# Performance work log

Measured on AMD Instinct MI355X. Metric: run time of the kernel, lower is better.

The kernel has to match this reference:

```python
import jax, jax.numpy as jnp
import numpy as np

N_NODES = 50000
N_EDGES = 800000


def setup_inputs() -> dict:
    key = jax.random.key(0)
    ks = jax.random.split(key, 8)
    x = jax.random.normal(ks[0], (N_NODES, 128), dtype=jnp.float32)
    edge_index = jax.random.randint(ks[1], (2, N_EDGES), 0, N_NODES, dtype=jnp.int32)
    # Glorot-ish scaled weights
    W1 = jax.random.normal(ks[2], (128, 64), dtype=jnp.float32) / np.sqrt(128.0)
    b1 = jnp.zeros((64,), dtype=jnp.float32)
    W2 = jax.random.normal(ks[3], (64, 64), dtype=jnp.float32) / np.sqrt(64.0)
    b2 = jnp.zeros((64,), dtype=jnp.float32)
    W3 = jax.random.normal(ks[4], (64, 32), dtype=jnp.float32) / np.sqrt(64.0)
    b3 = jnp.zeros((32,), dtype=jnp.float32)
    return {"x": x, "edge_index": edge_index, "W1": W1, "b1": b1,
            "W2": W2, "b2": b2, "W3": W3, "b3": b3}


def _gcn_norm(edge_index, n_nodes):
    """Add self-loops and compute symmetric GCN edge normalization."""
    loop = jnp.arange(n_nodes, dtype=edge_index.dtype)
    src = jnp.concatenate([edge_index[0], loop])  # [E+N]
    dst = jnp.concatenate([edge_index[1], loop])
    deg = jax.ops.segment_sum(jnp.ones_like(dst, dtype=jnp.float32), dst,
                              num_segments=n_nodes)
    dis = jax.lax.rsqrt(jnp.maximum(deg, 1.0))  # deg >= 1 due to self-loops
    norm = dis[src] * dis[dst]                  # [E+N]
    return src, dst, norm


def _gcn_conv(h, W, b, src, dst, norm, n_nodes):
    # transform-then-aggregate (PyG GCNConv): messages have out_channels dim
    h = h @ W                                   # [N, out]
    msg = h[src] * norm[:, None]                # [E+N, out] gather + scale
    out = jax.ops.segment_sum(msg, dst, num_segments=n_nodes)  # scatter-add
    return out + b


def reference(x, edge_index, W1, b1, W2, b2, W3, b3):
    n = x.shape[0]
    src, dst, norm = _gcn_norm(edge_index, n)
    h = jax.nn.relu(_gcn_conv(x, W1, b1, src, dst, norm, n))
    # dropout is identity in eval mode
    h = jax.nn.relu(_gcn_conv(h, W2, b2, src, dst, norm, n))
    out = _gcn_conv(h, W3, b3, src, dst, norm, n)
    return out
```

## Files before the change

kernel.cpp:

```cpp
#include <hip/hip_runtime.h>
#include <hip/hip_fp16.h>


#define P3CAP 3200
#define P4CAP 8192

typedef float vf4 __attribute__((ext_vector_type(4)));

__device__ __forceinline__ int block_scan_incl(int v, int* s, int t) {
    s[t] = v;
    __syncthreads();
#pragma unroll
    for (int d = 1; d < 256; d <<= 1) {
        int a = (t >= d) ? s[t - d] : 0;
        __syncthreads();
        s[t] += a;
        __syncthreads();
    }
    return s[t];
}

__host__ __device__ __forceinline__ int chunk_of(int E) {
    return (((E + 255) / 256) + 3) & ~3;
}

__global__ __launch_bounds__(256) void part_hist_kernel(
    const int* __restrict__ dst, int* __restrict__ hist, int E, int nbuckets)
{
    __shared__ int lh[256];
    const int t = threadIdx.x;
    lh[t] = 0;
    __syncthreads();
    const int chunk = chunk_of(E);
    const int e0 = blockIdx.x * chunk;
    const int e1 = min(E, e0 + chunk);
    int e = e0 + t * 4;
    for (; e + 3 < e1; e += 1024) {
        const int4 d4 = *(const int4*)&dst[e];
        atomicAdd(&lh[d4.x >> 8], 1);
        atomicAdd(&lh[d4.y >> 8], 1);
        atomicAdd(&lh[d4.z >> 8], 1);
        atomicAdd(&lh[d4.w >> 8], 1);
    }
    for (; e < e1; ++e) atomicAdd(&lh[dst[e] >> 8], 1);
    __syncthreads();
    if (t < nbuckets) hist[t * 256 + blockIdx.x] = lh[t];
}

__global__ __launch_bounds__(256) void part_scan_kernel(
    int* __restrict__ hist, int* __restrict__ btot)
{
    __shared__ int s[256];
    const int t = threadIdx.x;
    const int v = hist[blockIdx.x * 256 + t];
    const int inc = block_scan_incl(v, s, t);
    hist[blockIdx.x * 256 + t] = inc - v;
    if (t == 255) btot[blockIdx.x] = inc;
}

__global__ __launch_bounds__(256) void part_scatter_kernel(
    const int* __restrict__ src, const int* __restrict__ dst,
    const int* __restrict__ hist, const int* __restrict__ btot,
    int* __restrict__ bedge, int E, int nbuckets)
{
    __shared__ int lh[256], gb[256], cur[256], s[256];
    __shared__ int stage[P3CAP];
    const int t = threadIdx.x;

    const int bv = (t < nbuckets) ? btot[t] : 0;
    const int binc = block_scan_incl(bv, s, t);
    const int bbase_t = binc - bv;
    __syncthreads();

    lh[t] = 0;
    __syncthreads();
    const int chunk = chunk_of(E);
    const int e0 = blockIdx.x * chunk;
    const int e1 = min(E, e0 + chunk);
    {
        int e = e0 + t * 4;
        for (; e + 3 < e1; e += 1024) {
            const int4 d4 = *(const int4*)&dst[e];
            atomicAdd(&lh[d4.x >> 8], 1);
            atomicAdd(&lh[d4.y >> 8], 1);
            atomicAdd(&lh[d4.z >> 8], 1);
            atomicAdd(&lh[d4.w >> 8], 1);
        }
        for (; e < e1; ++e) atomicAdd(&lh[dst[e] >> 8], 1);
    }
    __syncthreads();
    const int v = lh[t];
    const int inc = block_scan_incl(v, s, t);
    const int excl = inc - v;
    cur[t] = excl;
    if (t < nbuckets) gb[t] = bbase_t + hist[t * 256 + blockIdx.x] - excl;
    __syncthreads();
    {
        int e = e0 + t * 4;
        for (; e + 3 < e1; e += 1024) {
            const int4 d4 = *(const int4*)&dst[e];
            const int4 s4 = *(const int4*)&src[e];
            int r, b;
            b = d4.x >> 8; r = atomicAdd(&cur[b], 1);
            stage[r] = (s4.x & 0xffff) | ((d4.x & 255) << 16) | (b << 24);
            b = d4.y >> 8; r = atomicAdd(&cur[b], 1);
            stage[r] = (s4.y & 0xffff) | ((d4.y & 255) << 16) | (b << 24);
            b = d4.z >> 8; r = atomicAdd(&cur[b], 1);
            stage[r] = (s4.z & 0xffff) | ((d4.z & 255) << 16) | (b << 24);
            b = d4.w >> 8; r = atomicAdd(&cur[b], 1);
            stage[r] = (s4.w & 0xffff) | ((d4.w & 255) << 16) | (b << 24);
        }
        for (; e < e1; ++e) {
            const int dv = dst[e];
            const int b = dv >> 8;
            const int r = atomicAdd(&cur[b], 1);
            stage[r] = (src[e] & 0xffff) | ((dv & 255) << 16) | (b << 24);
        }
    }
    __syncthreads();
    const int cnt = e1 - e0;
    for (int i = t; i < cnt; i += 256) {
        const int p = stage[i];
        const int bucket = (int)((unsigned)p >> 24);
        bedge[gb[bucket] + i] = p;
    }
}

__global__ __launch_bounds__(256) void bucket_csr_kernel(
    const int* __restrict__ bedge, const int* __restrict__ btot,
    int* __restrict__ csr, int* __restrict__ off, float* __restrict__ dis,
    int N, int nbuckets)
{
    __shared__ int deg[256], cur[256], s[256];
    __shared__ int e01[2];
    __shared__ int lcsr[P4CAP];
    const int t = threadIdx.x;
    const int b = blockIdx.x;

    const int bv = (t < nbuckets) ? btot[t] : 0;
    const int binc = block_scan_incl(bv, s, t);
    if (t == b) { e01[0] = binc - bv; e01[1] = binc; }
    __syncthreads();
    const int e0 = e01[0], e1 = e01[1];

    deg[t] = 0;
    __syncthreads();
    for (int e = e0 + t; e < e1; e += 256)
        atomicAdd(&deg[(bedge[e] >> 16) & 255], 1);
    __syncthreads();
    const int v = deg[t];
    const int inc = block_scan_incl(v, s, t);
    cur[t] = inc - v;
    const int node = (b << 8) + t;
    if (node < N) {
        off[node + 1] = e0 + inc;
        dis[node] = rsqrtf((float)v + 1.0f);
        if (node == 0) off[0] = 0;
    }
    __syncthreads();
    for (int e = e0 + t; e < e1; e += 256) {
        const int p = bedge[e];
        const int pos = atomicAdd(&cur[(p >> 16) & 255], 1);
        lcsr[pos] = p & 0xffff;
    }
    __syncthreads();
    for (int i = t; i < e1 - e0; i += 256)
        csr[e0 + i] = lcsr[i];
}

template<int K, int C, int TR>
__global__ __launch_bounds__(256) void gemm_scale_kernel(
    const float* __restrict__ in, const float* __restrict__ W,
    const float* __restrict__ dis, __half* __restrict__ hp, int N)
{
    constexpr int TX = C / 4;
    constexpr int R  = (256 / TX) * TR;
    __shared__ float Wl[K * C];

    const int t = threadIdx.x;
    for (int i = t; i < K * C / 4; i += 256)
        ((float4*)Wl)[i] = ((const float4*)W)[i];
    __syncthreads();

    const int tx = t % TX, ty = t / TX;
    const int cb = tx * 4;
    const int row0 = blockIdx.x * R + ty * TR;

    float acc[TR][4];
#pragma unroll
    for (int r = 0; r < TR; ++r) acc[r][0] = acc[r][1] = acc[r][2] = acc[r][3] = 0.0f;

    auto store_row = [&](int row, int r) {
        const float d = dis[row];
        __half2 h0 = __float22half2_rn(make_float2(acc[r][0] * d, acc[r][1] * d));
        __half2 h1 = __float22half2_rn(make_float2(acc[r][2] * d, acc[r][3] * d));
        uint2 u;
        u.x = *(unsigned*)&h0;
        u.y = *(unsigned*)&h1;
        *(uint2*)&hp[(size_t)row * C + cb] = u;
    };

    if (row0 + TR <= N) {
        const float* inp = in + (size_t)row0 * K;
#pragma unroll 4
        for (int k4 = 0; k4 < K / 4; ++k4) {
            float4 w0 = *(const float4*)&Wl[(k4 * 4 + 0) * C + cb];
            float4 w1 = *(const float4*)&Wl[(k4 * 4 + 1) * C + cb];
            float4 w2 = *(const float4*)&Wl[(k4 * 4 + 2) * C + cb];
            float4 w3 = *(const float4*)&Wl[(k4 * 4 + 3) * C + cb];
#pragma unroll
            for (int r = 0; r < TR; ++r) {
                const vf4 a = __builtin_nontemporal_load((const vf4*)&inp[r * K + k4 * 4]);
                acc[r][0] = fmaf(a.x, w0.x, acc[r][0]);
                acc[r][1] = fmaf(a.x, w0.y, acc[r][1]);
                acc[r][2] = fmaf(a.x, w0.z, acc[r][2]);
                acc[r][3] = fmaf(a.x, w0.w, acc[r][3]);
                acc[r][0] = fmaf(a.y, w1.x, acc[r][0]);
                acc[r][1] = fmaf(a.y, w1.y, acc[r][1]);
                acc[r][2] = fmaf(a.y, w1.z, acc[r][2]);
                acc[r][3] = fmaf(a.y, w1.w, acc[r][3]);
                acc[r][0] = fmaf(a.z, w2.x, acc[r][0]);
                acc[r][1] = fmaf(a.z, w2.y, acc[r][1]);
                acc[r][2] = fmaf(a.z, w2.z, acc[r][2]);
                acc[r][3] = fmaf(a.z, w2.w, acc[r][3]);
                acc[r][0] = fmaf(a.w, w3.x, acc[r][0]);
                acc[r][1] = fmaf(a.w, w3.y, acc[r][1]);
                acc[r][2] = fmaf(a.w, w3.z, acc[r][2]);
                acc[r][3] = fmaf(a.w, w3.w, acc[r][3]);
            }
        }
#pragma unroll
        for (int r = 0; r < TR; ++r) store_row(row0 + r, r);
    } else {
        for (int k = 0; k < K; ++k) {
            const float4 w4 = *(const float4*)&Wl[k * C + cb];
#pragma unroll
            for (int r = 0; r < TR; ++r) {
                const int row = row0 + r;
                const float a = (row < N) ? in[(size_t)row * K + k] : 0.0f;
                acc[r][0] = fmaf(a, w4.x, acc[r][0]);
                acc[r][1] = fmaf(a, w4.y, acc[r][1]);
                acc[r][2] = fmaf(a, w4.z, acc[r][2]);
                acc[r][3] = fmaf(a, w4.w, acc[r][3]);
            }
        }
#pragma unroll
        for (int r = 0; r < TR; ++r)
            if (row0 + r < N) store_row(row0 + r, r);
    }
}

template<int COUT>
__global__ __launch_bounds__(256) void fused_agg_gemm_kernel(
    const int* __restrict__ off, const int* __restrict__ csr,
    const float* __restrict__ dis, const __half* __restrict__ hp_in,
    const float* __restrict__ bias, const float* __restrict__ Wn,
    __half* __restrict__ hp_out, int N)
{
    constexpr int TX  = COUT / 4;
    constexpr int NPB = 256 / TX;
    constexpr int NPW = NPB / 4;
    __shared__ float Wl[64 * COUT];
    __shared__ float Al[NPB * 65];

    const int t = threadIdx.x;
    for (int i = t; i < 64 * COUT / 4; i += 256)
        ((float4*)Wl)[i] = ((const float4*)Wn)[i];

    const int wv   = t >> 6;
    const int lane = t & 63;
    const int grp  = lane >> 3;
    const int gl   = lane & 7;

    float b[8];
#pragma unroll
    for (int j = 0; j < 8; ++j) b[j] = bias[gl * 8 + j];

    auto accum = [](float4 v, float* a) {
        const __half2* h2 = (const __half2*)&v;
#pragma unroll
        for (int j = 0; j < 4; ++j) {
            const float2 pr = __half22float2(h2[j]);
            a[2 * j]     += pr.x;
            a[2 * j + 1] += pr.y;
        }
    };

    const int node0 = blockIdx.x * NPB + wv * NPW;
    for (int nl = 0; nl < NPW; ++nl) {
        const int node = node0 + nl;
        if (node >= N) break;
        const int s0 = off[node];
        const int s1 = off[node + 1];

        float acc[8]  = {0, 0, 0, 0, 0, 0, 0, 0};
        float acc2[8] = {0, 0, 0, 0, 0, 0, 0, 0};

        if (grp == 0) {
            const float4 v = *(const float4*)&hp_in[(size_t)node * 64 + gl * 8];
            accum(v, acc);
        }
        int e = s0 + grp;
        for (; e + 8 < s1; e += 16) {
            const int sa = csr[e];
            const int sb = csr[e + 8];
            const float4 va = *(const float4*)&hp_in[(size_t)sa * 64 + gl * 8];
            const float4 vb = *(const float4*)&hp_in[(size_t)sb * 64 + gl * 8];
            accum(va, acc);
            accum(vb, acc2);
        }
        if (e < s1) {
            const int sa = csr[e];
            const float4 va = *(const float4*)&hp_in[(size_t)sa * 64 + gl * 8];
            accum(va, acc);
        }
#pragma unroll
        for (int j = 0; j < 8; ++j) acc[j] += acc2[j];
#pragma unroll
        for (int d = 8; d < 64; d <<= 1) {
#pragma unroll
            for (int j = 0; j < 8; ++j) acc[j] += __shfl_xor(acc[j], d);
        }
        if (grp == 0) {
            const float dn = dis[node];
            const int row = wv * NPW + nl;
#pragma unroll
            for (int j = 0; j < 8; ++j)
                Al[row * 65 + gl * 8 + j] = fmaxf(fmaf(dn, acc[j], b[j]), 0.0f);
        }
    }
    __syncthreads();

    const int tx = t % TX, ty = t / TX;
    const int gnode = blockIdx.x * NPB + ty;
    const int cb = tx * 4;
    float c0 = 0.f, c1 = 0.f, c2 = 0.f, c3 = 0.f;
#pragma unroll 8
    for (int k = 0; k < 64; ++k) {
        const float a = Al[ty * 65 + k];
        const float4 w4 = *(const float4*)&Wl[k * COUT + cb];
        c0 = fmaf(a, w4.x, c0);
        c1 = fmaf(a, w4.y, c1);
        c2 = fmaf(a, w4.z, c2);
        c3 = fmaf(a, w4.w, c3);
    }
    if (gnode < N) {
        const float d = dis[gnode];
        __half2 h0 = __float22half2_rn(make_float2(c0 * d, c1 * d));
        __half2 h1 = __float22half2_rn(make_float2(c2 * d, c3 * d));
        uint2 u;
        u.x = *(unsigned*)&h0;
        u.y = *(unsigned*)&h1;
        *(uint2*)&hp_out[(size_t)gnode * COUT + cb] = u;
    }
}

template<int C, bool RELU>
__global__ __launch_bounds__(256) void agg_kernel(
    const int* __restrict__ off, const int* __restrict__ csr,
    const float* __restrict__ dis, const __half* __restrict__ hp,
    const float* __restrict__ bias, float* __restrict__ out, int N)
{
    constexpr int GL = C / 8;
    constexpr int G  = 64 / GL;
    const int wv   = threadIdx.x >> 6;
    const int lane = threadIdx.x & 63;
    const int grp  = lane / GL;
    const int gl   = lane % GL;
    const int node = blockIdx.x * 4 + wv;
    if (node >= N) return;

    const int s0 = off[node];
    const int s1 = off[node + 1];

    float acc[8]  = {0, 0, 0, 0, 0, 0, 0, 0};
    float acc2[8] = {0, 0, 0, 0, 0, 0, 0, 0};

    auto accum = [](float4 v, float* a) {
        const __half2* h2 = (const __half2*)&v;
#pragma unroll
        for (int j = 0; j < 4; ++j) {
            const float2 pr = __half22float2(h2[j]);
            a[2 * j]     += pr.x;
            a[2 * j + 1] += pr.y;
        }
    };

    if (grp == 0) {
        const float4 v = *(const float4*)&hp[(size_t)node * C + gl * 8];
        accum(v, acc);
    }
    int e = s0 + grp;
    for (; e + G < s1; e += 2 * G) {
        const int sa = csr[e];
        const int sb = csr[e + G];
        const float4 va = *(const float4*)&hp[(size_t)sa * C + gl * 8];
        const float4 vb = *(const float4*)&hp[(size_t)sb * C + gl * 8];
        accum(va, acc);
        accum(vb, acc2);
    }
    if (e < s1) {
        const int sa = csr[e];
        const float4 va = *(const float4*)&hp[(size_t)sa * C + gl * 8];
        accum(va, acc);
    }
#pragma unroll
    for (int j = 0; j < 8; ++j) acc[j] += acc2[j];

#pragma unroll
    for (int d = GL; d < 64; d <<= 1) {
#pragma unroll
        for (int j = 0; j < 8; ++j) acc[j] += __shfl_xor(acc[j], d);
    }

    if (grp == 0) {
        const float dn = dis[node];
        float v[8];
#pragma unroll
        for (int j = 0; j < 8; ++j) {
            v[j] = fmaf(dn, acc[j], bias[gl * 8 + j]);
            if (RELU) v[j] = fmaxf(v[j], 0.f);
        }
        *(float4*)&out[(size_t)node * C + gl * 8]     = make_float4(v[0], v[1], v[2], v[3]);
        *(float4*)&out[(size_t)node * C + gl * 8 + 4] = make_float4(v[4], v[5], v[6], v[7]);
    }
}

static inline size_t align_up(size_t x) { return (x + 255) & ~(size_t)255; }

extern "C" void kernel_launch(void* const* d_in, const int* in_sizes, int n_in,
                              void* d_out, int out_size, void* d_ws, size_t ws_size,
                              hipStream_t stream) {
    const float* x   = (const float*)d_in[0];
    const int*  eidx = (const int*)d_in[1];
    const float* W1  = (const float*)d_in[2];
    const float* b1  = (const float*)d_in[3];
    const float* W2  = (const float*)d_in[4];
    const float* b2  = (const float*)d_in[5];
    const float* W3  = (const float*)d_in[6];
    const float* b3  = (const float*)d_in[7];
    float* out = (float*)d_out;

    const int N = in_sizes[0] / 128;
    const int E = in_sizes[1] / 2;
    const int* srcp = eidx;
    const int* dstp = eidx + E;
    const int nbuckets = (N + 255) >> 8;

    char* ws = (char*)d_ws;
    size_t o = 0;
    float* dis   = (float*)(ws + o);  o = align_up(o + (size_t)N * 4);
    int* off     = (int*)(ws + o);    o = align_up(o + (size_t)(N + 1) * 4);
    int* btot    = (int*)(ws + o);    o = align_up(o + 256 * 4);
    int* hist    = (int*)(ws + o);    o = align_up(o + 256 * 256 * 4);
    int* bedge   = (int*)(ws + o);    o = align_up(o + (size_t)E * 4);
    int* csr     = (int*)(ws + o);    o = align_up(o + (size_t)E * 4);
    __half* H1   = (__half*)(ws + o); o = align_up(o + (size_t)N * 64 * 2);
    __half* H2   = (__half*)(ws + o); o = align_up(o + (size_t)N * 64 * 2);
    __half* H3   = H1;

    const dim3 blk(256);

    part_hist_kernel<<<dim3(256), blk, 0, stream>>>(dstp, hist, E, nbuckets);
    part_scan_kernel<<<dim3(nbuckets), blk, 0, stream>>>(hist, btot);
    part_scatter_kernel<<<dim3(256), blk, 0, stream>>>(srcp, dstp, hist, btot, bedge, E, nbuckets);
    bucket_csr_kernel<<<dim3(nbuckets), blk, 0, stream>>>(bedge, btot, csr, off, dis, N, nbuckets);

    gemm_scale_kernel<128, 64, 2><<<dim3((N + 31) / 32), blk, 0, stream>>>(x, W1, dis, H1, N);

    fused_agg_gemm_kernel<64><<<dim3((N + 15) / 16), blk, 0, stream>>>(
        off, csr, dis, H1, b1, W2, H2, N);

    fused_agg_gemm_kernel<32><<<dim3((N + 31) / 32), blk, 0, stream>>>(
        off, csr, dis, H2, b2, W3, H3, N);

    agg_kernel<32, false><<<dim3((N + 3) / 4), blk, 0, stream>>>(off, csr, dis, H3, b3, out, N);
}
```

Measured before the change: 215.0 us.

## Merge degree histogram with first GEMM and defer dis scaling to CSR build

The layer-1 GEMM no longer depends on the degree normalization. It now runs in the same launch as the partition histogram, with blocks beyond index 256 doing GEMM tiles. The per-row dis scaling of H1 moves into the bucket CSR kernel, which rescales its 256-row slice of H1 in place after computing degrees. The CSR kernel also stages its bucket edges in shared memory so they are not read from global memory twice. This removes one launch and overlaps the GEMM with the histogram, at the cost of an extra read-modify-write of H1, a second fp16 rounding, and more shared memory per CSR block.

After: 219.6 us. 1.02x slower.

```diff
diff --git a/kernel.cpp b/kernel.cpp
--- a/kernel.cpp
+++ b/kernel.cpp
@@ -24,60 +24,21 @@
     return (((E + 255) / 256) + 3) & ~3;
 }
 
-__global__ __launch_bounds__(256) void part_hist_kernel(
-    const int* __restrict__ dst, int* __restrict__ hist, int E, int nbuckets)
-{
-    __shared__ int lh[256];
+__global__ __launch_bounds__(256) void p1_gemm1_kernel(
+    const int* __restrict__ dst, int* __restrict__ hist, int E, int nbuckets,
+    const float* __restrict__ x, const float* __restrict__ W1,
+    __half* __restrict__ H1, int N)
+{
+    __shared__ __align__(16) char smem[32768];
     const int t = threadIdx.x;
-    lh[t] = 0;
-    __syncthreads();
-    const int chunk = chunk_of(E);
-    const int e0 = blockIdx.x * chunk;
-    const int e1 = min(E, e0 + chunk);
-    int e = e0 + t * 4;
-    for (; e + 3 < e1; e += 1024) {
-        const int4 d4 = *(const int4*)&dst[e];
-        atomicAdd(&lh[d4.x >> 8], 1);
-        atomicAdd(&lh[d4.y >> 8], 1);
-        atomicAdd(&lh[d4.z >> 8], 1);
-        atomicAdd(&lh[d4.w >> 8], 1);
-    }
-    for (; e < e1; ++e) atomicAdd(&lh[dst[e] >> 8], 1);
-    __syncthreads();
-    if (t < nbuckets) hist[t * 256 + blockIdx.x] = lh[t];
-}
-
-__global__ __launch_bounds__(256) void part_scan_kernel(
-    int* __restrict__ hist, int* __restrict__ btot)
-{
-    __shared__ int s[256];
-    const int t = threadIdx.x;
-    const int v = hist[blockIdx.x * 256 + t];
-    const int inc = block_scan_incl(v, s, t);
-    hist[blockIdx.x * 256 + t] = inc - v;
-    if (t == 255) btot[blockIdx.x] = inc;
-}
-
-__global__ __launch_bounds__(256) void part_scatter_kernel(
-    const int* __restrict__ src, const int* __restrict__ dst,
-    const int* __restrict__ hist, const int* __restrict__ btot,
-    int* __restrict__ bedge, int E, int nbuckets)
-{
-    __shared__ int lh[256], gb[256], cur[256], s[256];
-    __shared__ int stage[P3CAP];
-    const int t = threadIdx.x;
-
-    const int bv = (t < nbuckets) ? btot[t] : 0;
-    const int binc = block_scan_incl(bv, s, t);
-    const int bbase_t = binc - bv;
-    __syncthreads();
-
-    lh[t] = 0;
-    __syncthreads();
-    const int chunk = chunk_of(E);
-    const int e0 = blockIdx.x * chunk;
-    const int e1 = min(E, e0 + chunk);
-    {
+
+    if (blockIdx.x < 256) {
+        int* lh = (int*)smem;
+        lh[t] = 0;
+        __syncthreads();
+        const int chunk = chunk_of(E);
+        const int e0 = blockIdx.x * chunk;
+        const int e1 = min(E, e0 + chunk);
         int e = e0 + t * 4;
         for (; e + 3 < e1; e += 1024) {
             const int4 d4 = *(const int4*)&dst[e];
@@ -87,121 +48,38 @@
             atomicAdd(&lh[d4.w >> 8], 1);
         }
         for (; e < e1; ++e) atomicAdd(&lh[dst[e] >> 8], 1);
-    }
-    __syncthreads();
-    const int v = lh[t];
-    const int inc = block_scan_incl(v, s, t);
-    const int excl = inc - v;
-    cur[t] = excl;
-    if (t < nbuckets) gb[t] = bbase_t + hist[t * 256 + blockIdx.x] - excl;
-    __syncthreads();
-    {
-        int e = e0 + t * 4;
-        for (; e + 3 < e1; e += 1024) {
-            const int4 d4 = *(const int4*)&dst[e];
-            const int4 s4 = *(const int4*)&src[e];
-            int r, b;
-            b = d4.x >> 8; r = atomicAdd(&cur[b], 1);
-            stage[r] = (s4.x & 0xffff) | ((d4.x & 255) << 16) | (b << 24);
-            b = d4.y >> 8; r = atomicAdd(&cur[b], 1);
-            stage[r] = (s4.y & 0xffff) | ((d4.y & 255) << 16) | (b << 24);
-            b = d4.z >> 8; r = atomicAdd(&cur[b], 1);
-            stage[r] = (s4.z & 0xffff) | ((d4.z & 255) << 16) | (b << 24);
-            b = d4.w >> 8; r = atomicAdd(&cur[b], 1);
-            stage[r] = (s4.w & 0xffff) | ((d4.w & 255) << 16) | (b << 24);
-        }
-        for (; e < e1; ++e) {
-            const int dv = dst[e];
-            const int b = dv >> 8;
-            const int r = atomicAdd(&cur[b], 1);
-            stage[r] = (src[e] & 0xffff) | ((dv & 255) << 16) | (b << 24);
-        }
-    }
-    __syncthreads();
-    const int cnt = e1 - e0;
-    for (int i = t; i < cnt; i += 256) {
-        const int p = stage[i];
-        const int bucket = (int)((unsigned)p >> 24);
-        bedge[gb[bucket] + i] = p;
-    }
-}
-
-__global__ __launch_bounds__(256) void bucket_csr_kernel(
-    const int* __restrict__ bedge, const int* __restrict__ btot,
-    int* __restrict__ csr, int* __restrict__ off, float* __restrict__ dis,
-    int N, int nbuckets)
-{
-    __shared__ int deg[256], cur[256], s[256];
-    __shared__ int e01[2];
-    __shared__ int lcsr[P4CAP];
-    const int t = threadIdx.x;
-    const int b = blockIdx.x;
-
-    const int bv = (t < nbuckets) ? btot[t] : 0;
-    const int binc = block_scan_incl(bv, s, t);
-    if (t == b) { e01[0] = binc - bv; e01[1] = binc; }
-    __syncthreads();
-    const int e0 = e01[0], e1 = e01[1];
-
-    deg[t] = 0;
-    __syncthreads();
-    for (int e = e0 + t; e < e1; e += 256)
-        atomicAdd(&deg[(bedge[e] >> 16) & 255], 1);
-    __syncthreads();
-    const int v = deg[t];
-    const int inc = block_scan_incl(v, s, t);
-    cur[t] = inc - v;
-    const int node = (b << 8) + t;
-    if (node < N) {
-        off[node + 1] = e0 + inc;
-        dis[node] = rsqrtf((float)v + 1.0f);
-        if (node == 0) off[0] = 0;
-    }
-    __syncthreads();
-    for (int e = e0 + t; e < e1; e += 256) {
-        const int p = bedge[e];
-        const int pos = atomicAdd(&cur[(p >> 16) & 255], 1);
-        lcsr[pos] = p & 0xffff;
-    }
-    __syncthreads();
-    for (int i = t; i < e1 - e0; i += 256)
-        csr[e0 + i] = lcsr[i];
-}
-
-template<int K, int C, int TR>
-__global__ __launch_bounds__(256) void gemm_scale_kernel(
-    const float* __restrict__ in, const float* __restrict__ W,
-    const float* __restrict__ dis, __half* __restrict__ hp, int N)
-{
+        __syncthreads();
+        if (t < nbuckets) hist[t * 256 + blockIdx.x] = lh[t];
+        return;
+    }
+
+    constexpr int K = 128, C = 64, TR = 2;
     constexpr int TX = C / 4;
     constexpr int R  = (256 / TX) * TR;
-    __shared__ float Wl[K * C];
-
-    const int t = threadIdx.x;
+    float* Wl = (float*)smem;
     for (int i = t; i < K * C / 4; i += 256)
-        ((float4*)Wl)[i] = ((const float4*)W)[i];
+        ((float4*)Wl)[i] = ((const float4*)W1)[i];
     __syncthreads();
 
     const int tx = t % TX, ty = t / TX;
     const int cb = tx * 4;
-    const int row0 = blockIdx.x * R + ty * TR;
+    const int row0 = (blockIdx.x - 256) * R + ty * TR;
 
     float acc[TR][4];
 #pragma unroll
     for (int r = 0; r < TR; ++r) acc[r][0] = acc[r][1] = acc[r][2] = acc[r][3] = 0.0f;
 
     auto store_row = [&](int row, int r) {
-        const float d = dis[row];
-        __half2 h0 = __float22half2_rn(make_float2(acc[r][0] * d, acc[r][1] * d));
-        __half2 h1 = __float22half2_rn(make_float2(acc[r][2] * d, acc[r][3] * d));
+        __half2 h0 = __float22half2_rn(make_float2(acc[r][0], acc[r][1]));
+        __half2 h1 = __float22half2_rn(make_float2(acc[r][2], acc[r][3]));
         uint2 u;
         u.x = *(unsigned*)&h0;
         u.y = *(unsigned*)&h1;
-        *(uint2*)&hp[(size_t)row * C + cb] = u;
+        *(uint2*)&H1[(size_t)row * C + cb] = u;
     };
 
     if (row0 + TR <= N) {
-        const float* inp = in + (size_t)row0 * K;
+        const float* inp = x + (size_t)row0 * K;
 #pragma unroll 4
         for (int k4 = 0; k4 < K / 4; ++k4) {
             float4 w0 = *(const float4*)&Wl[(k4 * 4 + 0) * C + cb];
@@ -237,7 +115,7 @@
 #pragma unroll
             for (int r = 0; r < TR; ++r) {
                 const int row = row0 + r;
-                const float a = (row < N) ? in[(size_t)row * K + k] : 0.0f;
+                const float a = (row < N) ? x[(size_t)row * K + k] : 0.0f;
                 acc[r][0] = fmaf(a, w4.x, acc[r][0]);
                 acc[r][1] = fmaf(a, w4.y, acc[r][1]);
                 acc[r][2] = fmaf(a, w4.z, acc[r][2]);
@@ -247,6 +125,144 @@
 #pragma unroll
         for (int r = 0; r < TR; ++r)
             if (row0 + r < N) store_row(row0 + r, r);
+    }
+}
+
+__global__ __launch_bounds__(256) void part_scan_kernel(
+    int* __restrict__ hist, int* __restrict__ btot)
+{
+    __shared__ int s[256];
+    const int t = threadIdx.x;
+    const int v = hist[blockIdx.x * 256 + t];
+    const int inc = block_scan_incl(v, s, t);
+    hist[blockIdx.x * 256 + t] = inc - v;
+    if (t == 255) btot[blockIdx.x] = inc;
+}
+
+__global__ __launch_bounds__(256) void part_scatter_kernel(
+    const int* __restrict__ src, const int* __restrict__ dst,
+    const int* __restrict__ hist, const int* __restrict__ btot,
+    int* __restrict__ bedge, int E, int nbuckets)
+{
+    __shared__ int lh[256], gb[256], cur[256], s[256];
+    __shared__ int stage[P3CAP];
+    const int t = threadIdx.x;
+
+    const int bv = (t < nbuckets) ? btot[t] : 0;
+    const int binc = block_scan_incl(bv, s, t);
+    const int bbase_t = binc - bv;
+    __syncthreads();
+
+    lh[t] = 0;
+    __syncthreads();
+    const int chunk = chunk_of(E);
+    const int e0 = blockIdx.x * chunk;
+    const int e1 = min(E, e0 + chunk);
+    {
+        int e = e0 + t * 4;
+        for (; e + 3 < e1; e += 1024) {
+            const int4 d4 = *(const int4*)&dst[e];
+            atomicAdd(&lh[d4.x >> 8], 1);
+            atomicAdd(&lh[d4.y >> 8], 1);
+            atomicAdd(&lh[d4.z >> 8], 1);
+            atomicAdd(&lh[d4.w >> 8], 1);
+        }
+        for (; e < e1; ++e) atomicAdd(&lh[dst[e] >> 8], 1);
+    }
+    __syncthreads();
+    const int v = lh[t];
+    const int inc = block_scan_incl(v, s, t);
+    const int excl = inc - v;
+    cur[t] = excl;
+    if (t < nbuckets) gb[t] = bbase_t + hist[t * 256 + blockIdx.x] - excl;
+    __syncthreads();
+    {
+        int e = e0 + t * 4;
+        for (; e + 3 < e1; e += 1024) {
+            const int4 d4 = *(const int4*)&dst[e];
+            const int4 s4 = *(const int4*)&src[e];
+            int r, b;
+            b = d4.x >> 8; r = atomicAdd(&cur[b], 1);
+            stage[r] = (s4.x & 0xffff) | ((d4.x & 255) << 16) | (b << 24);
+            b = d4.y >> 8; r = atomicAdd(&cur[b], 1);
+            stage[r] = (s4.y & 0xffff) | ((d4.y & 255) << 16) | (b << 24);
+            b = d4.z >> 8; r = atomicAdd(&cur[b], 1);
+            stage[r] = (s4.z & 0xffff) | ((d4.z & 255) << 16) | (b << 24);
+            b = d4.w >> 8; r = atomicAdd(&cur[b], 1);
+            stage[r] = (s4.w & 0xffff) | ((d4.w & 255) << 16) | (b << 24);
+        }
+        for (; e < e1; ++e) {
+            const int dv = dst[e];
+            const int b = dv >> 8;
+            const int r = atomicAdd(&cur[b], 1);
+            stage[r] = (src[e] & 0xffff) | ((dv & 255) << 16) | (b << 24);
+        }
+    }
+    __syncthreads();
+    const int cnt = e1 - e0;
+    for (int i = t; i < cnt; i += 256) {
+        const int p = stage[i];
+        const int bucket = (int)((unsigned)p >> 24);
+        bedge[gb[bucket] + i] = p;
+    }
+}
+
+__global__ __launch_bounds__(256) void bucket_csr_kernel(
+    const int* __restrict__ bedge, const int* __restrict__ btot,
+    int* __restrict__ csr, int* __restrict__ off, float* __restrict__ dis,
+    __half* __restrict__ H1, int N, int nbuckets)
+{
+    __shared__ int deg[256], cur[256], s[256];
+    __shared__ float sdis[256];
+    __shared__ int e01[2];
+    __shared__ int ebuf[P4CAP];
+    __shared__ int lcsr[P4CAP];
+    const int t = threadIdx.x;
+    const int b = blockIdx.x;
+
+    const int bv = (t < nbuckets) ? btot[t] : 0;
+    const int binc = block_scan_incl(bv, s, t);
+    if (t == b) { e01[0] = binc - bv; e01[1] = binc; }
+    deg[t] = 0;
+    __syncthreads();
+    const int e0 = e01[0], e1 = e01[1];
+    const int m = e1 - e0;
+
+    for (int i = t; i < m; i += 256) ebuf[i] = bedge[e0 + i];
+    __syncthreads();
+    for (int i = t; i < m; i += 256)
+        atomicAdd(&deg[(ebuf[i] >> 16) & 255], 1);
+    __syncthreads();
+    const int v = deg[t];
+    const int inc = block_scan_incl(v, s, t);
+    cur[t] = inc - v;
+    const float dn = rsqrtf((float)v + 1.0f);
+    sdis[t] = dn;
+    const int node = (b << 8) + t;
+    if (node < N) {
+        off[node + 1] = e0 + inc;
+        dis[node] = dn;
+        if (node == 0) off[0] = 0;
+    }
+    __syncthreads();
+    for (int i = t; i < m; i += 256) {
+        const int p = ebuf[i];
+        const int pos = atomicAdd(&cur[(p >> 16) & 255], 1);
+        lcsr[pos] = p & 0xffff;
+    }
+    __syncthreads();
+    for (int i = t; i < m; i += 256)
+        csr[e0 + i] = lcsr[i];
+
+    const int nrows = min(256, N - (b << 8));
+    if (nrows > 0) {
+        __half2* Hh = (__half2*)H1;
+        const size_t hbase = (size_t)(b << 8) * 32;
+        for (int i = t; i < nrows * 32; i += 256) {
+            const float d2 = sdis[i >> 5];
+            const float2 f = __half22float2(Hh[hbase + i]);
+            Hh[hbase + i] = __float22half2_rn(make_float2(f.x * d2, f.y * d2));
+        }
     }
 }
 
@@ -460,19 +476,18 @@
     __half* H3   = H1;
 
     const dim3 blk(256);
-
-    part_hist_kernel<<<dim3(256), blk, 0, stream>>>(dstp, hist, E, nbuckets);
+    const int g1tiles = (N + 31) / 32;
+
+    p1_gemm1_kernel<<<dim3(256 + g1tiles), blk, 0, stream>>>(
+        dstp, hist, E, nbuckets, x, W1, H1, N);
     part_scan_kernel<<<dim3(nbuckets), blk, 0, stream>>>(hist, btot);
     part_scatter_kernel<<<dim3(256), blk, 0, stream>>>(srcp, dstp, hist, btot, bedge, E, nbuckets);
-    bucket_csr_kernel<<<dim3(nbuckets), blk, 0, stream>>>(bedge, btot, csr, off, dis, N, nbuckets);
-
-    gemm_scale_kernel<128, 64, 2><<<dim3((N + 31) / 32), blk, 0, stream>>>(x, W1, dis, H1, N);
+    bucket_csr_kernel<<<dim3(nbuckets), blk, 0, stream>>>(
+        bedge, btot, csr, off, dis, H1, N, nbuckets);
 
     fused_agg_gemm_kernel<64><<<dim3((N + 15) / 16), blk, 0, stream>>>(
         off, csr, dis, H1, b1, W2, H2, N);
-
     fused_agg_gemm_kernel<32><<<dim3((N + 31) / 32), blk, 0, stream>>>(
         off, csr, dis, H2, b2, W3, H3, N);
-
     agg_kernel<32, false><<<dim3((N + 3) / 4), blk, 0, stream>>>(off, csr, dis, H3, b3, out, N);
 }
```

## Interleave four nodes' gathers per wave and reuse histogram in scatter

Applied to the files above, without the earlier changes.

The aggregation kernels now process four destination nodes at once per wavefront, issuing independent neighbor gathers for all four before accumulating, which raises memory-level parallelism for the irregular gathers. The final aggregation is rewritten to handle 16 nodes per block with 4-lane groups per row. The partition scatter kernel reuses per-block histograms from the first pass instead of recounting them, and the scan writes its offsets to a separate buffer. The CSR build caches bucket edges in shared memory instead of reading them from global memory twice. In exchange, register pressure rises from the 4x8 accumulator arrays, and waves whose nodes have uneven degrees idle on the shorter lists.

Measured after the change: 247.9 us. +15.3%, slower.

```diff
diff --git a/kernel.cpp b/kernel.cpp
--- a/kernel.cpp
+++ b/kernel.cpp
@@ -48,22 +48,22 @@
 }
 
 __global__ __launch_bounds__(256) void part_scan_kernel(
-    int* __restrict__ hist, int* __restrict__ btot)
+    const int* __restrict__ hist, int* __restrict__ hoff, int* __restrict__ btot)
 {
     __shared__ int s[256];
     const int t = threadIdx.x;
     const int v = hist[blockIdx.x * 256 + t];
     const int inc = block_scan_incl(v, s, t);
-    hist[blockIdx.x * 256 + t] = inc - v;
+    hoff[blockIdx.x * 256 + t] = inc - v;
     if (t == 255) btot[blockIdx.x] = inc;
 }
 
 __global__ __launch_bounds__(256) void part_scatter_kernel(
     const int* __restrict__ src, const int* __restrict__ dst,
-    const int* __restrict__ hist, const int* __restrict__ btot,
-    int* __restrict__ bedge, int E, int nbuckets)
-{
-    __shared__ int lh[256], gb[256], cur[256], s[256];
+    const int* __restrict__ hist, const int* __restrict__ hoff,
+    const int* __restrict__ btot, int* __restrict__ bedge, int E, int nbuckets)
+{
+    __shared__ int gb[256], cur[256], s[256];
     __shared__ int stage[P3CAP];
     const int t = threadIdx.x;
 
@@ -72,29 +72,16 @@
     const int bbase_t = binc - bv;
     __syncthreads();
 
-    lh[t] = 0;
-    __syncthreads();
+    const int cnt_t = (t < nbuckets) ? hist[t * 256 + blockIdx.x] : 0;
+    const int inc = block_scan_incl(cnt_t, s, t);
+    const int excl = inc - cnt_t;
+    cur[t] = excl;
+    if (t < nbuckets) gb[t] = bbase_t + hoff[t * 256 + blockIdx.x] - excl;
+    __syncthreads();
+
     const int chunk = chunk_of(E);
     const int e0 = blockIdx.x * chunk;
     const int e1 = min(E, e0 + chunk);
-    {
-        int e = e0 + t * 4;
-        for (; e + 3 < e1; e += 1024) {
-            const int4 d4 = *(const int4*)&dst[e];
-            atomicAdd(&lh[d4.x >> 8], 1);
-            atomicAdd(&lh[d4.y >> 8], 1);
-            atomicAdd(&lh[d4.z >> 8], 1);
-            atomicAdd(&lh[d4.w >> 8], 1);
-        }
-        for (; e < e1; ++e) atomicAdd(&lh[dst[e] >> 8], 1);
-    }
-    __syncthreads();
-    const int v = lh[t];
-    const int inc = block_scan_incl(v, s, t);
-    const int excl = inc - v;
-    cur[t] = excl;
-    if (t < nbuckets) gb[t] = bbase_t + hist[t * 256 + blockIdx.x] - excl;
-    __syncthreads();
     {
         int e = e0 + t * 4;
         for (; e + 3 < e1; e += 1024) {
@@ -133,6 +120,7 @@
 {
     __shared__ int deg[256], cur[256], s[256];
     __shared__ int e01[2];
+    __shared__ int ebuf[P4CAP];
     __shared__ int lcsr[P4CAP];
     const int t = threadIdx.x;
     const int b = blockIdx.x;
@@ -140,13 +128,15 @@
     const int bv = (t < nbuckets) ? btot[t] : 0;
     const int binc = block_scan_incl(bv, s, t);
     if (t == b) { e01[0] = binc - bv; e01[1] = binc; }
+    deg[t] = 0;
     __syncthreads();
     const int e0 = e01[0], e1 = e01[1];
-
-    deg[t] = 0;
-    __syncthreads();
-    for (int e = e0 + t; e < e1; e += 256)
-        atomicAdd(&deg[(bedge[e] >> 16) & 255], 1);
+    const int m = e1 - e0;
+
+    for (int i = t; i < m; i += 256) ebuf[i] = bedge[e0 + i];
+    __syncthreads();
+    for (int i = t; i < m; i += 256)
+        atomicAdd(&deg[(ebuf[i] >> 16) & 255], 1);
     __syncthreads();
     const int v = deg[t];
     const int inc = block_scan_incl(v, s, t);
@@ -158,13 +148,13 @@
         if (node == 0) off[0] = 0;
     }
     __syncthreads();
-    for (int e = e0 + t; e < e1; e += 256) {
-        const int p = bedge[e];
+    for (int i = t; i < m; i += 256) {
+        const int p = ebuf[i];
         const int pos = atomicAdd(&cur[(p >> 16) & 255], 1);
         lcsr[pos] = p & 0xffff;
     }
     __syncthreads();
-    for (int i = t; i < e1 - e0; i += 256)
+    for (int i = t; i < m; i += 256)
         csr[e0 + i] = lcsr[i];
 }
 
@@ -250,6 +240,16 @@
     }
 }
 
+__device__ __forceinline__ void accum_h8(float4 v, float* a) {
+    const __half2* h2 = (const __half2*)&v;
+#pragma unroll
+    for (int j = 0; j < 4; ++j) {
+        const float2 pr = __half22float2(h2[j]);
+        a[2 * j]     += pr.x;
+        a[2 * j + 1] += pr.y;
+    }
+}
+
 template<int COUT>
 __global__ __launch_bounds__(256) void fused_agg_gemm_kernel(
     const int* __restrict__ off, const int* __restrict__ csr,
@@ -267,66 +267,72 @@
     for (int i = t; i < 64 * COUT / 4; i += 256)
         ((float4*)Wl)[i] = ((const float4*)Wn)[i];
 
-    const int wv   = t >> 6;
-    const int lane = t & 63;
-    const int grp  = lane >> 3;
-    const int gl   = lane & 7;
+    const int wv = t >> 6, lane = t & 63;
+    const int grp = lane >> 3, gl = lane & 7;
 
     float b[8];
 #pragma unroll
     for (int j = 0; j < 8; ++j) b[j] = bias[gl * 8 + j];
 
-    auto accum = [](float4 v, float* a) {
-        const __half2* h2 = (const __half2*)&v;
+    const int node0 = blockIdx.x * NPB + wv * NPW;
+
+    for (int pass = 0; pass < NPW; pass += 4) {
+        float acc[4][8];
+#pragma unroll
+        for (int j = 0; j < 4; ++j)
+#pragma unroll
+            for (int k = 0; k < 8; ++k) acc[j][k] = 0.0f;
+
+        int e_[4], e1_[4];
 #pragma unroll
         for (int j = 0; j < 4; ++j) {
-            const float2 pr = __half22float2(h2[j]);
-            a[2 * j]     += pr.x;
-            a[2 * j + 1] += pr.y;
-        }
-    };
-
-    const int node0 = blockIdx.x * NPB + wv * NPW;
-    for (int nl = 0; nl < NPW; ++nl) {
-        const int node = node0 + nl;
-        if (node >= N) break;
-        const int s0 = off[node];
-        const int s1 = off[node + 1];
-
-        float acc[8]  = {0, 0, 0, 0, 0, 0, 0, 0};
-        float acc2[8] = {0, 0, 0, 0, 0, 0, 0, 0};
-
-        if (grp == 0) {
-            const float4 v = *(const float4*)&hp_in[(size_t)node * 64 + gl * 8];
-            accum(v, acc);
-        }
-        int e = s0 + grp;
-        for (; e + 8 < s1; e += 16) {
-            const int sa = csr[e];
-            const int sb = csr[e + 8];
-            const float4 va = *(const float4*)&hp_in[(size_t)sa * 64 + gl * 8];
-            const float4 vb = *(const float4*)&hp_in[(size_t)sb * 64 + gl * 8];
-            accum(va, acc);
-            accum(vb, acc2);
-        }
-        if (e < s1) {
-            const int sa = csr[e];
-            const float4 va = *(const float4*)&hp_in[(size_t)sa * 64 + gl * 8];
-            accum(va, acc);
-        }
-#pragma unroll
-        for (int j = 0; j < 8; ++j) acc[j] += acc2[j];
-#pragma unroll
-        for (int d = 8; d < 64; d <<= 1) {
-#pragma unroll
-            for (int j = 0; j < 8; ++j) acc[j] += __shfl_xor(acc[j], d);
-        }
-        if (grp == 0) {
-            const float dn = dis[node];
-            const int row = wv * NPW + nl;
-#pragma unroll
-            for (int j = 0; j < 8; ++j)
-                Al[row * 65 + gl * 8 + j] = fmaxf(fmaf(dn, acc[j], b[j]), 0.0f);
+            const int node = node0 + pass + j;
+            if (node < N) {
+                e_[j]  = off[node] + grp;
+                e1_[j] = off[node + 1];
+                if (grp == 0) {
+                    const float4 v = *(const float4*)&hp_in[(size_t)node * 64 + gl * 8];
+                    accum_h8(v, acc[j]);
+                }
+            } else { e_[j] = 0; e1_[j] = 0; }
+        }
+
+        int more = 1;
+        while (more) {
+            more = 0;
+            float4 v[4];
+            bool ok[4];
+#pragma unroll
+            for (int j = 0; j < 4; ++j) {
+                ok[j] = (e_[j] < e1_[j]);
+                if (ok[j]) {
+                    const int sidx = csr[e_[j]];
+                    v[j] = *(const float4*)&hp_in[(size_t)sidx * 64 + gl * 8];
+                    e_[j] += 8;
+                    more = 1;
+                }
+            }
+#pragma unroll
+            for (int j = 0; j < 4; ++j)
+                if (ok[j]) accum_h8(v[j], acc[j]);
+        }
+
+#pragma unroll
+        for (int j = 0; j < 4; ++j) {
+#pragma unroll
+            for (int d = 8; d < 64; d <<= 1)
+#pragma unroll
+                for (int k = 0; k < 8; ++k) acc[j][k] += __shfl_xor(acc[j][k], d);
+            if (grp == 0) {
+                const int node = node0 + pass + j;
+                if (node < N) {
+                    const float dn = dis[node];
+                    const int row = wv * NPW + pass + j;
+#pragma unroll
+                    for (int k = 0; k < 8; ++k)
+                        Al[row * 65 + gl * 8 + k] = fmaxf(fmaf(dn, acc[j][k], b[k]), 0.0f);
+                }
+            }
         }
     }
     __syncthreads();
@@ -355,74 +361,74 @@
     }
 }
 
-template<int C, bool RELU>
-__global__ __launch_bounds__(256) void agg_kernel(
+__global__ __launch_bounds__(256) void agg3_kernel(
     const int* __restrict__ off, const int* __restrict__ csr,
     const float* __restrict__ dis, const __half* __restrict__ hp,
     const float* __restrict__ bias, float* __restrict__ out, int N)
 {
-    constexpr int GL = C / 8;
-    constexpr int G  = 64 / GL;
-    const int wv   = threadIdx.x >> 6;
-    const int lane = threadIdx.x & 63;
-    const int grp  = lane / GL;
-    const int gl   = lane % GL;
-    const int node = blockIdx.x * 4 + wv;
-    if (node >= N) return;
-
-    const int s0 = off[node];
-    const int s1 = off[node + 1];
-
-    float acc[8]  = {0, 0, 0, 0, 0, 0, 0, 0};
-    float acc2[8] = {0, 0, 0, 0, 0, 0, 0, 0};
-
-    auto accum = [](float4 v, float* a) {
-        const __half2* h2 = (const __half2*)&v;
+    const int t = threadIdx.x;
+    const int wv = t >> 6, lane = t & 63;
+    const int grp = lane >> 2, gl = lane & 3;
+    const int node0 = blockIdx.x * 16 + wv * 4;
+
+    float acc[4][8];
+#pragma unroll
+    for (int j = 0; j < 4; ++j)
+#pragma unroll
+        for (int k = 0; k < 8; ++k) acc[j][k] = 0.0f;
+
+    int e_[4], e1_[4];
+#pragma unroll
+    for (int j = 0; j < 4; ++j) {
+        const int node = node0 + j;
+        if (node < N) {
+            e_[j]  = off[node] + grp;
+            e1_[j] = off[node + 1];
+            if (grp == 0) {
+                const float4 v = *(const float4*)&hp[(size_t)node * 32 + gl * 8];
+                accum_h8(v, acc[j]);
+            }
+        } else { e_[j] = 0; e1_[j] = 0; }
+    }
+
+    int more = 1;
+    while (more) {
+        more = 0;
+        float4 v[4];
+        bool ok[4];
 #pragma unroll
         for (int j = 0; j < 4; ++j) {
-            const float2 pr = __half22float2(h2[j]);
-            a[2 * j]     += pr.x;
-            a[2 * j + 1] += pr.y;
-        }
-    };
-
-    if (grp == 0) {
-        const float4 v = *(const float4*)&hp[(size_t)node * C + gl * 8];
-        accum(v, acc);
-    }
-    int e = s0 + grp;
-    for (; e + G < s1; e += 2 * G) {
-        const int sa = csr[e];
-        const int sb = csr[e + G];
-        const float4 va = *(const float4*)&hp[(size_t)sa * C + gl * 8];
-        const float4 vb = *(const float4*)&hp[(size_t)sb * C + gl * 8];
-        accum(va, acc);
-        accum(vb, acc2);
-    }
-    if (e < s1) {
-        const int sa = csr[e];
-        const float4 va = *(const float4*)&hp[(size_t)sa * C + gl * 8];
-        accum(va, acc);
-    }
-#pragma unroll
-    for (int j = 0; j < 8; ++j) acc[j] += acc2[j];
-
-#pragma unroll
-    for (int d = GL; d < 64; d <<= 1) {
-#pragma unroll
-        for (int j = 0; j < 8; ++j) acc[j] += __shfl_xor(acc[j], d);
-    }
-
-    if (grp == 0) {
-        const float dn = dis[node];
-        float v[8];
-#pragma unroll
-        for (int j = 0; j < 8; ++j) {
-            v[j] = fmaf(dn, acc[j], bias[gl * 8 + j]);
-            if (RELU) v[j] = fmaxf(v[j], 0.f);
-        }
-        *(float4*)&out[(size_t)node * C + gl * 8]     = make_float4(v[0], v[1], v[2], v[3]);
-        *(float4*)&out[(size_t)node * C + gl * 8 + 4] = make_float4(v[4], v[5], v[6], v[7]);
+            ok[j] = (e_[j] < e1_[j]);
+            if (ok[j]) {
+                const int sidx = csr[e_[j]];
+                v[j] = *(const float4*)&hp[(size_t)sidx * 32 + gl * 8];
+                e_[j] += 16;
+                more = 1;
+            }
+        }
+#pragma unroll
+        for (int j = 0; j < 4; ++j)
+            if (ok[j]) accum_h8(v[j], acc[j]);
+    }
+
+#pragma unroll
+    for (int j = 0; j < 4; ++j) {
+#pragma unroll
+        for (int d = 4; d < 64; d <<= 1)
+#pragma unroll
+            for (int k = 0; k < 8; ++k) acc[j][k] += __shfl_xor(acc[j][k], d);
+        if (grp == 0) {
+            const int node = node0 + j;
+            if (node < N) {
+                const float dn = dis[node];
+                float v8[8];
+#pragma unroll
+                for (int k = 0; k < 8; ++k)
+                    v8[k] = fmaf(dn, acc[j][k], bias[gl * 8 + k]);
+                *(float4*)&out[(size_t)node * 32 + gl * 8]     = make_float4(v8[0], v8[1], v8[2], v8[3]);
+                *(float4*)&out[(size_t)node * 32 + gl * 8 + 4] = make_float4(v8[4], v8[5], v8[6], v8[7]);
+            }
+        }
     }
 }
 
@@ -453,6 +459,7 @@
     int* off     = (int*)(ws + o);    o = align_up(o + (size_t)(N + 1) * 4);
     int* btot    = (int*)(ws + o);    o = align_up(o + 256 * 4);
     int* hist    = (int*)(ws + o);    o = align_up(o + 256 * 256 * 4);
+    int* hoff    = (int*)(ws + o);    o = align_up(o + 256 * 256 * 4);
     int* bedge   = (int*)(ws + o);    o = align_up(o + (size_t)E * 4);
     int* csr     = (int*)(ws + o);    o = align_up(o + (size_t)E * 4);
     __half* H1   = (__half*)(ws + o); o = align_up(o + (size_t)N * 64 * 2);
@@ -462,17 +469,15 @@
     const dim3 blk(256);
 
     part_hist_kernel<<<dim3(256), blk, 0, stream>>>(dstp, hist, E, nbuckets);
-    part_scan_kernel<<<dim3(nbuckets), blk, 0, stream>>>(hist, btot);
-    part_scatter_kernel<<<dim3(256), blk, 0, stream>>>(srcp, dstp, hist, btot, bedge, E, nbuckets);
+    part_scan_kernel<<<dim3(nbuckets), blk, 0, stream>>>(hist, hoff, btot);
+    part_scatter_kernel<<<dim3(256), blk, 0, stream>>>(srcp, dstp, hist, hoff, btot, bedge, E, nbuckets);
     bucket_csr_kernel<<<dim3(nbuckets), blk, 0, stream>>>(bedge, btot, csr, off, dis, N, nbuckets);
 
     gemm_scale_kernel<128, 64, 2><<<dim3((N + 31) / 32), blk, 0, stream>>>(x, W1, dis, H1, N);
 
     fused_agg_gemm_kernel<64><<<dim3((N + 15) / 16), blk, 0, stream>>>(
         off, csr, dis, H1, b1, W2, H2, N);
-
     fused_agg_gemm_kernel<32><<<dim3((N + 31) / 32), blk, 0, stream>>>(
         off, csr, dis, H2, b2, W3, H3, N);
-
-    agg_kernel<32, false><<<dim3((N + 3) / 4), blk, 0, stream>>>(off, csr, dis, H3, b3, out, N);
-}
+    agg3_kernel<<<dim3((N + 15) / 16), blk, 0, stream>>>(off, csr, dis, H3, b3, out, N);
+}
```
